# Optimization experiments

Hardware: AMD Instinct MI355X
Metric: run time of the kernel (lower is better)

## Reference

```python
import jax, jax.numpy as jnp
import numpy as np

B, C, H, W = 8, 256, 64, 64
AGENT = 5
SCALE = C ** -0.5


def setup_inputs() -> dict:
    key = jax.random.key(0)
    ks = jax.random.split(key, 10)
    d = {}
    d["supp_feat1"] = jax.random.normal(ks[0], (B, C, H, W), jnp.float32)
    d["supp_feat2"] = jax.random.normal(ks[1], (B, C, H, W), jnp.float32)
    d["supp_mask1"] = jax.random.randint(ks[2], (B, H, W), 0, 2, jnp.int32)
    d["supp_mask2"] = jax.random.randint(ks[3], (B, H, W), 0, 2, jnp.int32)
    d["query_feat"] = jax.random.normal(ks[4], (B, C, H, W), jnp.float32)
    d["query_prediction"] = jax.random.normal(ks[5], (B, 2, H, W), jnp.float32)
    d["Wq"] = jax.random.normal(ks[6], (C, C), jnp.float32) * 0.02
    d["Wk"] = jax.random.normal(ks[7], (C, C), jnp.float32) * 0.02
    d["Wv"] = jax.random.normal(ks[8], (C, C), jnp.float32) * 0.02
    d["part_tokens"] = jax.random.normal(ks[9], (1, AGENT, C), jnp.float32) * 0.001
    return d


def _sinkhorn_masked(cost, col_mask, reg=0.5, n_iter=300):
    # Masked-column Sinkhorn equivalent to ot.sinkhorn on the fg-selected
    # submatrix (uniform marginals), then zero-scattered back. cost: [r, c].
    r = cost.shape[0]
    a = jnp.full((r,), 1.0 / r, cost.dtype)
    b = col_mask / jnp.sum(col_mask)          # 0 on masked cols
    K = jnp.exp(-cost / reg) * col_mask        # kill masked cols

    def body(u, _):
        v = b / jnp.maximum(K.T @ u, 1e-30)
        u_new = a / jnp.maximum(K @ v, 1e-30)
        return u_new, None

    u, _ = jax.lax.scan(body, a, None, length=n_iter)
    v = b / jnp.maximum(K.T @ u, 1e-30)
    return u[:, None] * K * v[None, :]         # transport plan [r, c]


def _supp_to_prototype(feat, mask, Wq, Wk, Wv, part_tokens):
    # mask is at feature resolution, so F.interpolate is identity.
    mf = (mask == 1).astype(feat.dtype)[:, None]                  # [B,1,H,W]
    proto = jnp.sum(feat * mf, axis=(2, 3)) / (jnp.sum(mf, axis=(2, 3)) + 1e-5)  # [B,C]
    proto = proto[:, None, :] + part_tokens                       # [B,A,C]
    q = proto @ Wq.T                                              # [B,A,C]
    sf = (feat * mf).reshape(B, C, H * W).transpose(0, 2, 1)      # [B,HW,C]
    k = sf @ Wk.T
    v = sf @ Wv.T
    attn = jnp.einsum("bac,bnc->ban", q, k)                      # [B,A,HW]
    # torch does (~mask_int).float() * -1e4 == (mask_int + 1) * 1e4
    bias = (mask.reshape(B, -1) + 1).astype(feat.dtype) * 10000.0
    attn = jax.nn.softmax(attn + bias[:, None, :], axis=-1)
    # background cols are exp(-1e4) == 0 in fp32, so attn > 0 <=> mask == 1
    col_mask = (mask.reshape(B, -1) == 1).astype(feat.dtype)      # [B,HW]
    cost = 1.0 - attn                                             # detached in torch
    plan = jax.lax.stop_gradient(jax.vmap(_sinkhorn_masked)(cost, col_mask))
    return proto + jnp.einsum("ban,bnc->bac", plan, v)


def _forward(supp_feat1, supp_feat2, supp_mask1, supp_mask2, query_feat,
             query_prediction, Wq, Wk, Wv, part_tokens):
    p1 = _supp_to_prototype(supp_feat1, supp_mask1, Wq, Wk, Wv, part_tokens)
    p2 = _supp_to_prototype(supp_feat2, supp_mask2, Wq, Wk, Wv, part_tokens)
    curr = jnp.concatenate([p1, p2], axis=1)                      # [B,2A,C]
    fg = jax.nn.softmax(query_prediction, axis=1)[:, 1:2]         # [B,1,H,W]
    fg = jnp.where(fg > 0.7, jnp.asarray(1.0, fg.dtype), fg)
    fg = jnp.where(fg < 0.3, jnp.asarray(0.0, fg.dtype), fg)
    qf = (query_feat * fg).reshape(B, C, H * W).transpose(0, 2, 1)  # [B,HW,C]
    attn = jnp.einsum("bnc,bmc->bnm", curr, qf) * SCALE
    attn = jax.nn.softmax(attn, axis=-1)
    curr = curr + jnp.einsum("bnm,bmc->bnc", attn, qf)
    mem = jnp.concatenate([p1, p2, curr], axis=1)                 # [B,4A,C]
    curr_prototype = jnp.mean(mem, axis=1, keepdims=True)         # [B,1,C]
    return mem, curr_prototype


def reference(supp_feat1, supp_feat2, supp_mask1, supp_mask2, query_feat,
              query_prediction, Wq, Wk, Wv, part_tokens):
    return _forward(supp_feat1, supp_feat2, supp_mask1, supp_mask2, query_feat,
                    query_prediction, Wq, Wk, Wv, part_tokens)
```

## Files before the change

kernel.cpp:

```cpp
#include <hip/hip_runtime.h>
#include <hip/hip_bf16.h>
#include <math.h>

#define HW 4096
#define NC 256
#define NB 8
#define NA 5
#define NIT 24
#define SCL 0.0625f

#define OFF_A     0
#define OFF_PROTO 655360
#define OFF_PS    (OFF_PROTO + 4096 + 20480)
#define OFF_W2    (OFF_PS + 20480)
#define OFF_WQK   OFF_W2

__device__ inline float frcp(float x) { return __builtin_amdgcn_rcpf(x); }

template<int NV>
__device__ inline void waveSum(float (&v)[NV]) {
    #pragma unroll
    for (int k = 0; k < NV; ++k) {
        float x = v[k]; int t;
        t = __builtin_amdgcn_update_dpp(0, __float_as_int(x), 0x111, 0xf, 0xf, true); x += __int_as_float(t);
        t = __builtin_amdgcn_update_dpp(0, __float_as_int(x), 0x112, 0xf, 0xf, true); x += __int_as_float(t);
        t = __builtin_amdgcn_update_dpp(0, __float_as_int(x), 0x114, 0xf, 0xf, true); x += __int_as_float(t);
        t = __builtin_amdgcn_update_dpp(0, __float_as_int(x), 0x118, 0xf, 0xf, true); x += __int_as_float(t);
        t = __builtin_amdgcn_update_dpp(0, __float_as_int(x), 0x142, 0xf, 0xf, true); x += __int_as_float(t);
        t = __builtin_amdgcn_update_dpp(0, __float_as_int(x), 0x143, 0xf, 0xf, true); x += __int_as_float(t);
        v[k] = x;
    }
}

template<int NV>
__device__ inline void waveMax(float (&v)[NV]) {
    #pragma unroll
    for (int k = 0; k < NV; ++k) {
        float x = v[k]; int t;
        t = __builtin_amdgcn_update_dpp(__float_as_int(x), __float_as_int(x), 0x111, 0xf, 0xf, false); x = fmaxf(x, __int_as_float(t));
        t = __builtin_amdgcn_update_dpp(__float_as_int(x), __float_as_int(x), 0x112, 0xf, 0xf, false); x = fmaxf(x, __int_as_float(t));
        t = __builtin_amdgcn_update_dpp(__float_as_int(x), __float_as_int(x), 0x114, 0xf, 0xf, false); x = fmaxf(x, __int_as_float(t));
        t = __builtin_amdgcn_update_dpp(__float_as_int(x), __float_as_int(x), 0x118, 0xf, 0xf, false); x = fmaxf(x, __int_as_float(t));
        t = __builtin_amdgcn_update_dpp(__float_as_int(x), __float_as_int(x), 0x142, 0xf, 0xf, false); x = fmaxf(x, __int_as_float(t));
        t = __builtin_amdgcn_update_dpp(__float_as_int(x), __float_as_int(x), 0x143, 0xf, 0xf, false); x = fmaxf(x, __int_as_float(t));
        v[k] = x;
    }
}

template<int NV>
__device__ inline void crossSum4(float (&v)[NV], float* buf, int lane, int wid) {
    waveSum<NV>(v);
    if (lane == 63) {
        #pragma unroll
        for (int k = 0; k < NV; ++k) buf[wid * NV + k] = v[k];
    }
    __syncthreads();
    #pragma unroll
    for (int k = 0; k < NV; ++k)
        v[k] = buf[k] + buf[NV + k] + buf[2 * NV + k] + buf[3 * NV + k];
}

template<int NV>
__device__ inline void crossMax4(float (&v)[NV], float* buf, int lane, int wid) {
    waveMax<NV>(v);
    if (lane == 63) {
        #pragma unroll
        for (int k = 0; k < NV; ++k) buf[wid * NV + k] = v[k];
    }
    __syncthreads();
    #pragma unroll
    for (int k = 0; k < NV; ++k)
        v[k] = fmaxf(fmaxf(buf[k], buf[NV + k]), fmaxf(buf[2 * NV + k], buf[3 * NV + k]));
}

__global__ __launch_bounds__(256) void k_stage1(const float* __restrict__ f1, const float* __restrict__ f2,
                                                const int* __restrict__ m1, const int* __restrict__ m2,
                                                const float* __restrict__ Wq, const float* __restrict__ Wk,
                                                float* __restrict__ ws) {
    __shared__ float buf[12];
    int bid = blockIdx.x, tid = threadIdx.x;
    if (bid < 2048) {
        int lane = tid & 63, wid = tid >> 6;
        int s = bid >> 10, b = (bid >> 7) & 7, cp = bid & 127;
        int c0 = cp * 2;
        const float* f = s ? f2 : f1;
        const int* m = s ? m2 : m1;
        const float4* r0 = (const float4*)(f + ((size_t)b * NC + c0) * HW);
        const float4* r1 = (const float4*)(f + ((size_t)b * NC + c0 + 1) * HW);
        const int4* mb4 = (const int4*)(m + b * HW);
        float v3[3] = {0.f, 0.f, 0.f};
        #pragma unroll
        for (int j = 0; j < 4; ++j) {
            int idx = tid + j * 256;
            float4 a = r0[idx];
            float4 c = r1[idx];
            int4 mm = mb4[idx];
            if (mm.x == 1) { v3[0] += a.x; v3[1] += c.x; v3[2] += 1.f; }
            if (mm.y == 1) { v3[0] += a.y; v3[1] += c.y; v3[2] += 1.f; }
            if (mm.z == 1) { v3[0] += a.z; v3[1] += c.z; v3[2] += 1.f; }
            if (mm.w == 1) { v3[0] += a.w; v3[1] += c.w; v3[2] += 1.f; }
        }
        crossSum4<3>(v3, buf, lane, wid);
        if (tid == 0) {
            float inv = 1.f / (v3[2] + 1e-5f);
            float* p = ws + OFF_PROTO + (s * 8 + b) * NC + c0;
            p[0] = v3[0] * inv;
            p[1] = v3[1] * inv;
        }
    } else {
        int c1 = bid - 2048;
        float acc = 0.f;
        #pragma unroll 8
        for (int cp = 0; cp < NC; ++cp)
            acc += Wq[(size_t)cp * NC + c1] * Wk[(size_t)cp * NC + tid];
        ws[OFF_WQK + (size_t)c1 * NC + tid] = acc;
    }
}

__global__ __launch_bounds__(256) void k_attnlogF(const float* __restrict__ f1, const float* __restrict__ f2,
                                                  const float* __restrict__ tok, float* __restrict__ ws) {
    __shared__ float sp3[NA * NC];
    __shared__ float qk_l[NA * NC];
    int bid = blockIdx.x, tid = threadIdx.x;
    int nt = bid & 15, sb = bid >> 4;
    int s = sb >> 3, b = sb & 7;
    const float* f = s ? f2 : f1;
    const float* proto = ws + OFF_PROTO + sb * NC;
    for (int i = tid; i < NA * NC; i += 256) sp3[i] = proto[i & 255] + tok[i];
    __syncthreads();
    {
        const float* wq = ws + OFF_WQK + tid;
        float a0 = 0, a1 = 0, a2 = 0, a3 = 0, a4 = 0;
        #pragma unroll 8
        for (int ci = 0; ci < NC; ++ci) {
            float w = wq[(size_t)ci * NC];
            a0 += sp3[0 * NC + ci] * w; a1 += sp3[1 * NC + ci] * w; a2 += sp3[2 * NC + ci] * w;
            a3 += sp3[3 * NC + ci] * w; a4 += sp3[4 * NC + ci] * w;
        }
        qk_l[0 * NC + tid] = a0; qk_l[1 * NC + tid] = a1; qk_l[2 * NC + tid] = a2;
        qk_l[3 * NC + tid] = a3; qk_l[4 * NC + tid] = a4;
    }
    __syncthreads();
    int n = nt * 256 + tid;
    const float* fb = f + (size_t)b * NC * HW + n;
    float acc[NA] = {};
    #pragma unroll 4
    for (int c = 0; c < NC; ++c) {
        float v = fb[(size_t)c * HW];
        #pragma unroll
        for (int a = 0; a < NA; ++a) acc[a] += qk_l[a * NC + c] * v;
    }
    float* Lb = ws + OFF_A + (size_t)sb * NA * HW;
    #pragma unroll
    for (int a = 0; a < NA; ++a) Lb[a * HW + n] = acc[a];
}

__global__ __launch_bounds__(256) void k_sinkhorn(const int* __restrict__ m1, const int* __restrict__ m2,
                                                  float* __restrict__ ws) {
    __shared__ float buf[2][24];
    int sb = blockIdx.x, tid = threadIdx.x;
    int lane = tid & 63, wid = tid >> 6;
    int s = sb >> 3, b = sb & 7;
    const int* m = (s ? m2 : m1) + b * HW;
    const float4* A4 = (const float4*)(ws + OFF_A) + (size_t)sb * NA * 1024;
    const int4* mb4 = (const int4*)m;

    unsigned mbits = 0;
    float K[NA][16];
    #pragma unroll
    for (int j = 0; j < 4; ++j) {
        int idx = tid + j * 256;
        int4 mm = mb4[idx];
        if (mm.x == 1) mbits |= 1u << (4 * j + 0);
        if (mm.y == 1) mbits |= 1u << (4 * j + 1);
        if (mm.z == 1) mbits |= 1u << (4 * j + 2);
        if (mm.w == 1) mbits |= 1u << (4 * j + 3);
        #pragma unroll
        for (int a = 0; a < NA; ++a) {
            float4 l0 = A4[a * 1024 + idx];
            K[a][4 * j + 0] = l0.x; K[a][4 * j + 1] = l0.y;
            K[a][4 * j + 2] = l0.z; K[a][4 * j + 3] = l0.w;
        }
    }
    float r[NA];
    #pragma unroll
    for (int a = 0; a < NA; ++a) {
        float mx = -3.0e38f;
        #pragma unroll
        for (int j = 0; j < 16; ++j)
            if ((mbits >> j) & 1) mx = fmaxf(mx, K[a][j]);
        r[a] = mx;
    }
    crossMax4<NA>(r, buf[0], lane, wid);
    float rs6[6];
    #pragma unroll
    for (int a = 0; a < NA; ++a) {
        float sum = 0.f;
        #pragma unroll
        for (int j = 0; j < 16; ++j) {
            float e = ((mbits >> j) & 1) ? expf(K[a][j] - r[a]) : 0.f;
            K[a][j] = e; sum += e;
        }
        rs6[a] = sum;
    }
    rs6[5] = (float)__popc(mbits);
    crossSum4<6>(rs6, buf[1], lane, wid);
    float inv_cnt = frcp(rs6[5]);
    #pragma unroll
    for (int a = 0; a < NA; ++a) {
        float irs = frcp(rs6[a]);
        #pragma unroll
        for (int j = 0; j < 16; ++j) {
            float attn = K[a][j] * irs;
            K[a][j] = ((mbits >> j) & 1) ? expf(2.f * attn - 2.f) : 0.f;
        }
    }
    float u[NA];
    #pragma unroll
    for (int a = 0; a < NA; ++a) u[a] = 0.2f;
    for (int it = 0; it < NIT; ++it) {
        float part[NA] = {0, 0, 0, 0, 0};
        #pragma unroll
        for (int j = 0; j < 16; ++j) {
            float d = 0.f;
            #pragma unroll
            for (int a = 0; a < NA; ++a) d += K[a][j] * u[a];
            float t = inv_cnt * frcp(fmaxf(d, 1e-30f));
            #pragma unroll
            for (int a = 0; a < NA; ++a) part[a] += K[a][j] * t;
        }
        crossSum4<NA>(part, buf[it & 1], lane, wid);
        #pragma unroll
        for (int a = 0; a < NA; ++a) u[a] = 0.2f * frcp(fmaxf(part[a], 1e-30f));
    }
    float4* Pb4 = (float4*)(ws + OFF_A) + (size_t)sb * NA * 1024;
    #pragma unroll
    for (int j4 = 0; j4 < 4; ++j4) {
        int idx = tid + j4 * 256;
        float tcol[4];
        #pragma unroll
        for (int k = 0; k < 4; ++k) {
            int j = 4 * j4 + k;
            float d = 0.f;
            #pragma unroll
            for (int a = 0; a < NA; ++a) d += K[a][j] * u[a];
            tcol[k] = inv_cnt * frcp(fmaxf(d, 1e-30f));
        }
        #pragma unroll
        for (int a = 0; a < NA; ++a) {
            float4 o;
            o.x = u[a] * K[a][4 * j4 + 0] * tcol[0];
            o.y = u[a] * K[a][4 * j4 + 1] * tcol[1];
            o.z = u[a] * K[a][4 * j4 + 2] * tcol[2];
            o.w = u[a] * K[a][4 * j4 + 3] * tcol[3];
            Pb4[a * 1024 + idx] = o;
        }
    }
}

__global__ __launch_bounds__(256) void k_ps(const float* __restrict__ f1, const float* __restrict__ f2,
                                            float* __restrict__ ws) {
    __shared__ float buf[20];
    int bid = blockIdx.x, tid = threadIdx.x;
    int lane = tid & 63, wid = tid >> 6;
    int s = bid >> 11, b = (bid >> 8) & 7, c = bid & 255;
    const float* f = s ? f2 : f1;
    int sb = s * 8 + b;
    const float4* fb4 = (const float4*)(f + ((size_t)b * NC + c) * HW);
    const float4* Pb4 = (const float4*)(ws + OFF_A) + (size_t)sb * NA * 1024;
    float acc[NA] = {0, 0, 0, 0, 0};
    #pragma unroll
    for (int j = 0; j < 4; ++j) {
        int idx = tid + j * 256;
        float4 v = fb4[idx];
        #pragma unroll
        for (int a = 0; a < NA; ++a) {
            float4 p = Pb4[a * 1024 + idx];
            acc[a] += p.x * v.x + p.y * v.y + p.z * v.z + p.w * v.w;
        }
    }
    crossSum4<NA>(acc, buf, lane, wid);
    if (tid == 0) {
        float* ps = ws + OFF_PS + sb * NA * NC;
        #pragma unroll
        for (int a = 0; a < NA; ++a) ps[a * NC + c] = acc[a];
    }
}

__global__ __launch_bounds__(256) void k_outproto(const float* __restrict__ Wv, const float* __restrict__ tok,
                                                  float* __restrict__ ws, float* __restrict__ out) {
    __shared__ float wv_l[16][NC + 1];
    __shared__ float ps_l[NA * NC];
    __shared__ float part[80][2];
    int bid = blockIdx.x, tid = threadIdx.x;
    int ctile = bid & 15, sb = bid >> 4;
    int s = sb >> 3, b = sb & 7;
    int c0 = ctile * 16;
    const float4* wv4 = (const float4*)(Wv + (size_t)c0 * NC);
    for (int t = tid; t < 1024; t += 256) {
        int r = t >> 6, q = t & 63;
        float4 v = wv4[(size_t)r * 64 + q];
        wv_l[r][4 * q + 0] = v.x; wv_l[r][4 * q + 1] = v.y;
        wv_l[r][4 * q + 2] = v.z; wv_l[r][4 * q + 3] = v.w;
    }
    const float* ps = ws + OFF_PS + sb * NA * NC;
    for (int i = tid; i < NA * NC; i += 256) ps_l[i] = ps[i];
    __syncthreads();
    if (tid < 160) {
        int o = tid >> 1, seg = tid & 1;
        int a = o >> 4, r = o & 15;
        const float* pa = ps_l + a * NC + seg * 128;
        const float* wr = &wv_l[r][seg * 128];
        float d = 0.f;
        #pragma unroll 8
        for (int i = 0; i < 128; ++i) d += pa[i] * wr[i];
        part[o][seg] = d;
    }
    __syncthreads();
    if (tid < 80) {
        int a = tid >> 4, r = tid & 15;
        int c = c0 + r;
        out[(size_t)b * 20 * NC + (s * NA + a) * NC + c] =
            ws[OFF_PROTO + sb * NC + c] + tok[a * NC + c] + part[tid][0] + part[tid][1];
    }
}

__global__ __launch_bounds__(256) void k_attn2log(const float* __restrict__ qf, const float* __restrict__ out,
                                                  float* __restrict__ ws) {
    int bid = blockIdx.x, tid = threadIdx.x;
    int ct = bid & 1, nt = (bid >> 1) & 7, b = bid >> 4;
    const float* cw = out + (size_t)b * 20 * NC + ct * 128;
    int h0 = nt * 256 + tid;
    const float2* fb2 = (const float2*)(qf + (size_t)b * NC * HW + (size_t)ct * 128 * HW);
    float2 acc[10] = {};
    #pragma unroll 2
    for (int k = 0; k < 128; ++k) {
        float2 v = fb2[(size_t)k * 2048 + h0];
        #pragma unroll
        for (int i = 0; i < 10; ++i) {
            float w = cw[i * NC + k];
            acc[i].x += w * v.x; acc[i].y += w * v.y;
        }
    }
    float2* pp = (float2*)(ws + OFF_A + (size_t)((ct * 8 + b) * 10) * HW);
    #pragma unroll
    for (int i = 0; i < 10; ++i) pp[(size_t)i * 2048 + h0] = acc[i];
}

__global__ __launch_bounds__(256) void k_softmax2(const float* __restrict__ qp, float* __restrict__ ws) {
    __shared__ float buf[2][8];
    int row = blockIdx.x, tid = threadIdx.x;
    int lane = tid & 63, wid = tid >> 6;
    int b = row / 10, i = row - b * 10;
    const float4* pA = (const float4*)(ws + OFF_A) + (size_t)(b * 10 + i) * 1024;
    const float4* pB = (const float4*)(ws + OFF_A) + (size_t)((8 + b) * 10 + i) * 1024;
    const float4* qp0 = (const float4*)(qp + (size_t)b * 2 * HW);
    const float4* qp1 = qp0 + 1024;
    float4 lg[4], fgv[4];
    float mx[1] = {-3.0e38f};
    #pragma unroll
    for (int j = 0; j < 4; ++j) {
        int idx = tid + j * 256;
        float4 a = pA[idx], c = pB[idx];
        float4 p0 = qp0[idx], p1 = qp1[idx];
        float4 fg;
        fg.x = 1.f / (1.f + expf(p0.x - p1.x));
        fg.y = 1.f / (1.f + expf(p0.y - p1.y));
        fg.z = 1.f / (1.f + expf(p0.z - p1.z));
        fg.w = 1.f / (1.f + expf(p0.w - p1.w));
        fg.x = fg.x > 0.7f ? 1.f : (fg.x < 0.3f ? 0.f : fg.x);
        fg.y = fg.y > 0.7f ? 1.f : (fg.y < 0.3f ? 0.f : fg.y);
        fg.z = fg.z > 0.7f ? 1.f : (fg.z < 0.3f ? 0.f : fg.z);
        fg.w = fg.w > 0.7f ? 1.f : (fg.w < 0.3f ? 0.f : fg.w);
        fgv[j] = fg;
        lg[j].x = (a.x + c.x) * SCL * fg.x;
        lg[j].y = (a.y + c.y) * SCL * fg.y;
        lg[j].z = (a.z + c.z) * SCL * fg.z;
        lg[j].w = (a.w + c.w) * SCL * fg.w;
        mx[0] = fmaxf(mx[0], fmaxf(fmaxf(lg[j].x, lg[j].y), fmaxf(lg[j].z, lg[j].w)));
    }
    crossMax4<1>(mx, buf[0], lane, wid);
    float sum[1] = {0.f};
    #pragma unroll
    for (int j = 0; j < 4; ++j) {
        lg[j].x = expf(lg[j].x - mx[0]); lg[j].y = expf(lg[j].y - mx[0]);
        lg[j].z = expf(lg[j].z - mx[0]); lg[j].w = expf(lg[j].w - mx[0]);
        sum[0] += lg[j].x + lg[j].y + lg[j].z + lg[j].w;
    }
    crossSum4<1>(sum, buf[1], lane, wid);
    float inv = frcp(sum[0]);
    float4* w24 = (float4*)(ws + OFF_W2) + (size_t)row * 1024;
    #pragma unroll
    for (int j = 0; j < 4; ++j) {
        int idx = tid + j * 256;
        float4 o;
        o.x = lg[j].x * inv * fgv[j].x;
        o.y = lg[j].y * inv * fgv[j].y;
        o.z = lg[j].z * inv * fgv[j].z;
        o.w = lg[j].w * inv * fgv[j].w;
        w24[idx] = o;
    }
}

__global__ __launch_bounds__(256) void k_apply2(const float* __restrict__ qf, float* __restrict__ ws,
                                                float* __restrict__ out) {
    __shared__ float buf[4 * 40];
    int bid = blockIdx.x, tid = threadIdx.x;
    int lane = tid & 63, wid = tid >> 6;
    int b = bid >> 6, cg = bid & 63;
    int c0 = cg * 4;
    const float4* qf4 = (const float4*)(qf + (size_t)b * NC * HW);
    const float4* w24 = (const float4*)(ws + OFF_W2) + (size_t)b * 10 * 1024;
    float acc[40] = {};
    #pragma unroll
    for (int j = 0; j < 4; ++j) {
        int idx = tid + j * 256;
        float4 wv[10];
        #pragma unroll
        for (int i = 0; i < 10; ++i) wv[i] = w24[i * 1024 + idx];
        #pragma unroll
        for (int cc = 0; cc < 4; ++cc) {
            float4 v = qf4[(size_t)(c0 + cc) * 1024 + idx];
            #pragma unroll
            for (int i = 0; i < 10; ++i)
                acc[cc * 10 + i] += wv[i].x * v.x + wv[i].y * v.y + wv[i].z * v.z + wv[i].w * v.w;
        }
    }
    waveSum<40>(acc);
    if (lane == 63) {
        #pragma unroll
        for (int k = 0; k < 40; ++k) buf[wid * 40 + k] = acc[k];
    }
    __syncthreads();
    if (tid == 0) {
        float* ob = out + (size_t)b * 20 * NC;
        #pragma unroll
        for (int cc = 0; cc < 4; ++cc) {
            float s = 0.f;
            #pragma unroll
            for (int i = 0; i < 10; ++i) {
                float d = buf[cc * 10 + i] + buf[40 + cc * 10 + i]
                        + buf[80 + cc * 10 + i] + buf[120 + cc * 10 + i];
                float base = ob[i * NC + c0 + cc];
                float r = base + d;
                ob[(10 + i) * NC + c0 + cc] = r;
                s += base + r;
            }
            out[40960 + b * NC + c0 + cc] = s * 0.05f;
        }
    }
}

extern "C" void kernel_launch(void* const* d_in, const int* in_sizes, int n_in,
                              void* d_out, int out_size, void* d_ws, size_t ws_size,
                              hipStream_t stream) {
    const float* f1  = (const float*)d_in[0];
    const float* f2  = (const float*)d_in[1];
    const int*   m1  = (const int*)d_in[2];
    const int*   m2  = (const int*)d_in[3];
    const float* qf  = (const float*)d_in[4];
    const float* qp  = (const float*)d_in[5];
    const float* Wq  = (const float*)d_in[6];
    const float* Wk  = (const float*)d_in[7];
    const float* Wv  = (const float*)d_in[8];
    const float* tok = (const float*)d_in[9];
    float* out = (float*)d_out;
    float* ws  = (float*)d_ws;

    k_stage1<<<2304, 256, 0, stream>>>(f1, f2, m1, m2, Wq, Wk, ws);
    k_attnlogF<<<256, 256, 0, stream>>>(f1, f2, tok, ws);
    k_sinkhorn<<<16, 256, 0, stream>>>(m1, m2, ws);
    k_ps<<<4096, 256, 0, stream>>>(f1, f2, ws);
    k_outproto<<<256, 256, 0, stream>>>(Wv, tok, ws, out);
    k_attn2log<<<128, 256, 0, stream>>>(qf, out, ws);
    k_softmax2<<<80, 256, 0, stream>>>(qp, ws);
    k_apply2<<<512, 256, 0, stream>>>(qf, ws, out);
}
```

Measured before the change: 151.0 us.

## Split channel reduction across four waves-groups in attention logit kernels

Both logit kernels (support attention and query attention) now launch 1024-thread blocks. Each 256-thread group reduces a quarter of the channel dimension, and the partial sums are combined in shared memory. The query-attention kernel now splits over prototype groups instead of channel halves, so the softmax kernel reads a single precomputed logit instead of adding two partials. The aim is more in-flight memory parallelism and occupancy for these bandwidth-bound reductions, at the cost of extra shared-memory traffic and block-level synchronisation.

```diff
diff --git a/kernel.cpp b/kernel.cpp
--- a/kernel.cpp
+++ b/kernel.cpp
@@ -117,42 +117,62 @@
     }
 }
 
-__global__ __launch_bounds__(256) void k_attnlogF(const float* __restrict__ f1, const float* __restrict__ f2,
-                                                  const float* __restrict__ tok, float* __restrict__ ws) {
+__global__ __launch_bounds__(1024) void k_attnlogF(const float* __restrict__ f1, const float* __restrict__ f2,
+                                                   const float* __restrict__ tok, float* __restrict__ ws) {
     __shared__ float sp3[NA * NC];
     __shared__ float qk_l[NA * NC];
+    __shared__ float red[4 * NA * 256];
     int bid = blockIdx.x, tid = threadIdx.x;
     int nt = bid & 15, sb = bid >> 4;
     int s = sb >> 3, b = sb & 7;
     const float* f = s ? f2 : f1;
     const float* proto = ws + OFF_PROTO + sb * NC;
-    for (int i = tid; i < NA * NC; i += 256) sp3[i] = proto[i & 255] + tok[i];
-    __syncthreads();
+    for (int i = tid; i < NA * NC; i += 1024) sp3[i] = proto[i & 255] + tok[i];
+    __syncthreads();
+    int g = tid >> 8, t8 = tid & 255;
     {
-        const float* wq = ws + OFF_WQK + tid;
+        const float* wq = ws + OFF_WQK + (size_t)(g * 64) * NC + t8;
         float a0 = 0, a1 = 0, a2 = 0, a3 = 0, a4 = 0;
         #pragma unroll 8
-        for (int ci = 0; ci < NC; ++ci) {
+        for (int ci = 0; ci < 64; ++ci) {
             float w = wq[(size_t)ci * NC];
-            a0 += sp3[0 * NC + ci] * w; a1 += sp3[1 * NC + ci] * w; a2 += sp3[2 * NC + ci] * w;
-            a3 += sp3[3 * NC + ci] * w; a4 += sp3[4 * NC + ci] * w;
-        }
-        qk_l[0 * NC + tid] = a0; qk_l[1 * NC + tid] = a1; qk_l[2 * NC + tid] = a2;
-        qk_l[3 * NC + tid] = a3; qk_l[4 * NC + tid] = a4;
-    }
-    __syncthreads();
-    int n = nt * 256 + tid;
+            int cix = g * 64 + ci;
+            a0 += sp3[0 * NC + cix] * w; a1 += sp3[1 * NC + cix] * w; a2 += sp3[2 * NC + cix] * w;
+            a3 += sp3[3 * NC + cix] * w; a4 += sp3[4 * NC + cix] * w;
+        }
+        red[(g * NA + 0) * 256 + t8] = a0; red[(g * NA + 1) * 256 + t8] = a1;
+        red[(g * NA + 2) * 256 + t8] = a2; red[(g * NA + 3) * 256 + t8] = a3;
+        red[(g * NA + 4) * 256 + t8] = a4;
+    }
+    __syncthreads();
+    for (int o = tid; o < NA * 256; o += 1024) {
+        int j = o >> 8, c = o & 255;
+        qk_l[j * NC + c] = red[(0 * NA + j) * 256 + c] + red[(1 * NA + j) * 256 + c]
+                         + red[(2 * NA + j) * 256 + c] + red[(3 * NA + j) * 256 + c];
+    }
+    __syncthreads();
+    int n = nt * 256 + t8;
     const float* fb = f + (size_t)b * NC * HW + n;
-    float acc[NA] = {};
-    #pragma unroll 4
-    for (int c = 0; c < NC; ++c) {
-        float v = fb[(size_t)c * HW];
-        #pragma unroll
-        for (int a = 0; a < NA; ++a) acc[a] += qk_l[a * NC + c] * v;
-    }
+    {
+        float acc[NA] = {};
+        #pragma unroll 4
+        for (int k = 0; k < 64; ++k) {
+            int c = g * 64 + k;
+            float v = fb[(size_t)c * HW];
+            #pragma unroll
+            for (int a = 0; a < NA; ++a) acc[a] += qk_l[a * NC + c] * v;
+        }
+        #pragma unroll
+        for (int a = 0; a < NA; ++a) red[(g * NA + a) * 256 + t8] = acc[a];
+    }
+    __syncthreads();
     float* Lb = ws + OFF_A + (size_t)sb * NA * HW;
-    #pragma unroll
-    for (int a = 0; a < NA; ++a) Lb[a * HW + n] = acc[a];
+    for (int o = tid; o < NA * 256; o += 1024) {
+        int j = o >> 8, c = o & 255;
+        Lb[(size_t)j * HW + nt * 256 + c] =
+            red[(0 * NA + j) * 256 + c] + red[(1 * NA + j) * 256 + c]
+          + red[(2 * NA + j) * 256 + c] + red[(3 * NA + j) * 256 + c];
+    }
 }
 
 __global__ __launch_bounds__(256) void k_sinkhorn(const int* __restrict__ m1, const int* __restrict__ m2,
@@ -325,26 +345,38 @@
     }
 }
 
-__global__ __launch_bounds__(256) void k_attn2log(const float* __restrict__ qf, const float* __restrict__ out,
-                                                  float* __restrict__ ws) {
+__global__ __launch_bounds__(1024) void k_attn2log(const float* __restrict__ qf, const float* __restrict__ out,
+                                                   float* __restrict__ ws) {
+    __shared__ float sc_l[NA * NC];
+    __shared__ float red[4 * NA * 256];
     int bid = blockIdx.x, tid = threadIdx.x;
-    int ct = bid & 1, nt = (bid >> 1) & 7, b = bid >> 4;
-    const float* cw = out + (size_t)b * 20 * NC + ct * 128;
-    int h0 = nt * 256 + tid;
-    const float2* fb2 = (const float2*)(qf + (size_t)b * NC * HW + (size_t)ct * 128 * HW);
-    float2 acc[10] = {};
-    #pragma unroll 2
-    for (int k = 0; k < 128; ++k) {
-        float2 v = fb2[(size_t)k * 2048 + h0];
-        #pragma unroll
-        for (int i = 0; i < 10; ++i) {
-            float w = cw[i * NC + k];
-            acc[i].x += w * v.x; acc[i].y += w * v.y;
-        }
-    }
-    float2* pp = (float2*)(ws + OFF_A + (size_t)((ct * 8 + b) * 10) * HW);
-    #pragma unroll
-    for (int i = 0; i < 10; ++i) pp[(size_t)i * 2048 + h0] = acc[i];
+    int ig = bid & 1, nt = (bid >> 1) & 15, b = bid >> 5;
+    const float* cb = out + (size_t)b * 20 * NC + ig * NA * NC;
+    for (int i = tid; i < NA * NC; i += 1024) sc_l[i] = cb[i];
+    __syncthreads();
+    int g = tid >> 8, t8 = tid & 255;
+    int n = nt * 256 + t8;
+    const float* fb = qf + (size_t)b * NC * HW + n;
+    {
+        float acc[NA] = {};
+        #pragma unroll 4
+        for (int k = 0; k < 64; ++k) {
+            int c = g * 64 + k;
+            float v = fb[(size_t)c * HW];
+            #pragma unroll
+            for (int a = 0; a < NA; ++a) acc[a] += sc_l[a * NC + c] * v;
+        }
+        #pragma unroll
+        for (int a = 0; a < NA; ++a) red[(g * NA + a) * 256 + t8] = acc[a];
+    }
+    __syncthreads();
+    float* pp = ws + OFF_A + (size_t)((ig * 8 + b) * NA) * HW;
+    for (int o = tid; o < NA * 256; o += 1024) {
+        int j = o >> 8, c = o & 255;
+        pp[(size_t)j * HW + nt * 256 + c] =
+            red[(0 * NA + j) * 256 + c] + red[(1 * NA + j) * 256 + c]
+          + red[(2 * NA + j) * 256 + c] + red[(3 * NA + j) * 256 + c];
+    }
 }
 
 __global__ __launch_bounds__(256) void k_softmax2(const float* __restrict__ qp, float* __restrict__ ws) {
@@ -352,8 +384,8 @@
     int row = blockIdx.x, tid = threadIdx.x;
     int lane = tid & 63, wid = tid >> 6;
     int b = row / 10, i = row - b * 10;
-    const float4* pA = (const float4*)(ws + OFF_A) + (size_t)(b * 10 + i) * 1024;
-    const float4* pB = (const float4*)(ws + OFF_A) + (size_t)((8 + b) * 10 + i) * 1024;
+    int ig = i / NA, ii = i - ig * NA;
+    const float4* pA = (const float4*)(ws + OFF_A) + (size_t)((ig * 8 + b) * NA + ii) * 1024;
     const float4* qp0 = (const float4*)(qp + (size_t)b * 2 * HW);
     const float4* qp1 = qp0 + 1024;
     float4 lg[4], fgv[4];
@@ -361,7 +393,7 @@
     #pragma unroll
     for (int j = 0; j < 4; ++j) {
         int idx = tid + j * 256;
-        float4 a = pA[idx], c = pB[idx];
+        float4 a = pA[idx];
         float4 p0 = qp0[idx], p1 = qp1[idx];
         float4 fg;
         fg.x = 1.f / (1.f + expf(p0.x - p1.x));
@@ -373,10 +405,10 @@
         fg.z = fg.z > 0.7f ? 1.f : (fg.z < 0.3f ? 0.f : fg.z);
         fg.w = fg.w > 0.7f ? 1.f : (fg.w < 0.3f ? 0.f : fg.w);
         fgv[j] = fg;
-        lg[j].x = (a.x + c.x) * SCL * fg.x;
-        lg[j].y = (a.y + c.y) * SCL * fg.y;
-        lg[j].z = (a.z + c.z) * SCL * fg.z;
-        lg[j].w = (a.w + c.w) * SCL * fg.w;
+        lg[j].x = a.x * SCL * fg.x;
+        lg[j].y = a.y * SCL * fg.y;
+        lg[j].z = a.z * SCL * fg.z;
+        lg[j].w = a.w * SCL * fg.w;
         mx[0] = fmaxf(mx[0], fmaxf(fmaxf(lg[j].x, lg[j].y), fmaxf(lg[j].z, lg[j].w)));
     }
     crossMax4<1>(mx, buf[0], lane, wid);
@@ -468,11 +500,11 @@
     float* ws  = (float*)d_ws;
 
     k_stage1<<<2304, 256, 0, stream>>>(f1, f2, m1, m2, Wq, Wk, ws);
-    k_attnlogF<<<256, 256, 0, stream>>>(f1, f2, tok, ws);
+    k_attnlogF<<<256, 1024, 0, stream>>>(f1, f2, tok, ws);
     k_sinkhorn<<<16, 256, 0, stream>>>(m1, m2, ws);
     k_ps<<<4096, 256, 0, stream>>>(f1, f2, ws);
     k_outproto<<<256, 256, 0, stream>>>(Wv, tok, ws, out);
-    k_attn2log<<<128, 256, 0, stream>>>(qf, out, ws);
+    k_attn2log<<<256, 1024, 0, stream>>>(qf, out, ws);
     k_softmax2<<<80, 256, 0, stream>>>(qp, ws);
     k_apply2<<<512, 256, 0, stream>>>(qf, ws, out);
 }
```

New measurement: 126.6 us. 16.2% less time.
